# Optimization experiments

Hardware: AMD Instinct MI355X
Metric: run time of the kernel (lower is better)

The kernel has to match this reference:

```python
import jax, jax.numpy as jnp
import numpy as np
from jax import lax

DIM = 192
HEADS = 8
WIN = 16
B, H, W = 4, 256, 256


def setup_inputs() -> dict:
    key = jax.random.key(0)
    ks = jax.random.split(key, 8)
    s = 0.02
    return {
        "x": jax.random.normal(ks[0], (B, H, W, DIM), dtype=jnp.float32),
        "ln_g": jnp.ones((DIM,), jnp.float32),
        "ln_b": jnp.zeros((DIM,), jnp.float32),
        "wq1": jax.random.normal(ks[1], (DIM, DIM), jnp.float32) * s,
        "wq2": jax.random.normal(ks[2], (DIM, 1, 3, 3), jnp.float32) * s,
        "wk1": jax.random.normal(ks[3], (DIM, DIM), jnp.float32) * s,
        "wk2": jax.random.normal(ks[4], (DIM, 1, 3, 3), jnp.float32) * s,
        "wv1": jax.random.normal(ks[5], (DIM, DIM), jnp.float32) * s,
        "wv2": jax.random.normal(ks[6], (DIM, 1, 3, 3), jnp.float32) * s,
        "rescale": jnp.ones((HEADS, 1, 1), jnp.float32),
        "w_out": jax.random.normal(ks[7], (DIM, DIM), jnp.float32) * s,
    }


def _layernorm(x, g, b, eps=1e-5):
    mu = jnp.mean(x, axis=-1, keepdims=True)
    var = jnp.var(x, axis=-1, keepdims=True)
    return (x - mu) * lax.rsqrt(var + eps) * g + b


def _qkv(x_nchw, w1, w2):
    # 1x1 pointwise conv (no bias) as GEMM, then 3x3 depthwise conv (groups=dim)
    y = jnp.einsum('oi,bihw->bohw', w1, x_nchw)
    return lax.conv_general_dilated(
        y, w2, window_strides=(1, 1), padding='SAME',
        feature_group_count=DIM,
        dimension_numbers=('NCHW', 'OIHW', 'NCHW'))


def _windows(t):
    # [b,c,H,W] -> [b, nW, heads, d, n]   (nW = num_h*num_w, n = Wh*Ww)
    b = t.shape[0]
    nh, nw = H // WIN, W // WIN
    t = t.reshape(b, DIM, nh, WIN, nw, WIN)
    t = t.transpose(0, 1, 2, 4, 3, 5).reshape(b, DIM, nh * nw, WIN * WIN)
    d = DIM // HEADS
    t = t.reshape(b, HEADS, d, nh * nw, WIN * WIN)
    return t.transpose(0, 3, 1, 2, 4)  # b N h d n


def reference(x, ln_g, ln_b, wq1, wq2, wk1, wk2, wv1, wv2, rescale, w_out):
    b, h, w, c = x.shape
    xn = _layernorm(x, ln_g, ln_b)
    xc = xn.transpose(0, 3, 1, 2)  # NCHW
    q = _windows(_qkv(xc, wq1, wq2))
    k = _windows(_qkv(xc, wk1, wk2))
    v = _windows(_qkv(xc, wv1, wv2))
    # spectral (channel-wise) attention inside each window
    sim = jnp.einsum('bNhin,bNhjn->bNhij', q, k) * rescale
    attn = jax.nn.softmax(sim, axis=-1)
    out = jnp.einsum('bNhij,bNhjn->bNhin', attn, v)  # [b,N,h,d,n]
    # merge heads, un-window
    nh, nw = h // WIN, w // WIN
    out = out.transpose(0, 2, 3, 1, 4).reshape(b, c, nh * nw, WIN * WIN)
    out = out.reshape(b, c, nh, nw, WIN, WIN).transpose(0, 1, 2, 4, 3, 5).reshape(b, c, h, w)
    out = jnp.einsum('oi,bihw->bohw', w_out, out)
    return out.transpose(0, 2, 3, 1)  # [b,h,w,c]
```

## Files before the change

### kernel.cpp

```cpp
#include <hip/hip_runtime.h>
#include <hip/hip_bf16.h>

#define CH    192
#define NB    4
#define NHH   256
#define NWW   256
#define NPOS  (NB*NHH*NWW)
#define HEADS 8
#define DH    24
#define WIN   16
#define PS    ((size_t)NPOS*DH)

typedef unsigned short u16;
typedef __bf16 bf16x8 __attribute__((ext_vector_type(8)));
typedef float  f32x4  __attribute__((ext_vector_type(4)));
typedef u16    u16x8  __attribute__((ext_vector_type(8)));
typedef u16    u16x4  __attribute__((ext_vector_type(4)));

__device__ __forceinline__ float b2f(u16 h) {
    union { unsigned int u; float f; } x; x.u = ((unsigned int)h) << 16; return x.f;
}
__device__ __forceinline__ u16 f2b(float f) {
    union { float f; unsigned int u; } x; x.f = f;
    return (u16)((x.u + 0x7fffu + ((x.u >> 16) & 1u)) >> 16);
}

__global__ __launch_bounds__(256) void prep_weights(
    const float* __restrict__ w0, const float* __restrict__ w1,
    const float* __restrict__ w2, const float* __restrict__ w3,
    u16* __restrict__ pack)
{
    const int t = blockIdx.x * 256 + threadIdx.x;
    const int lane = t & 63, g = t >> 6;
    const int mat = g / 72;
    const float* w = (mat == 0) ? w0 : (mat == 1) ? w1 : (mat == 2) ? w2 : w3;
    const int nt = (g / 6) % 12, ks = g % 6;
    const float* src = w + (nt*16 + (lane & 15)) * CH + ks*32 + (lane >> 4) * 8;
    const float4 a = *(const float4*)(src);
    const float4 b = *(const float4*)(src + 4);
    u16x8 o;
    o[0]=f2b(a.x); o[1]=f2b(a.y); o[2]=f2b(a.z); o[3]=f2b(a.w);
    o[4]=f2b(b.x); o[5]=f2b(b.y); o[6]=f2b(b.z); o[7]=f2b(b.w);
    *(u16x8*)(pack + (size_t)g*512 + lane*8) = o;
}

__global__ __launch_bounds__(256) void ln_qkv_gemm(
    const float* __restrict__ x, const float* __restrict__ lng, const float* __restrict__ lnb,
    const u16* __restrict__ bpack,
    u16* __restrict__ y0, u16* __restrict__ y1, u16* __restrict__ y2)
{
    __shared__ __align__(16) u16 At[64*192];
    __shared__ __align__(16) u16 St32[32*200];
    const int t = threadIdx.x, l = t & 63, w = t >> 6;
    const int lr = l & 15, lg = l >> 4;
    const size_t p0 = (size_t)blockIdx.x * 64;

    {
        const int row = t >> 2, part = t & 3;
        const float* xp = x + (p0 + row) * CH + part * 48;
        float vals[48];
#pragma unroll
        for (int j = 0; j < 12; ++j) {
            float4 v4 = *(const float4*)(xp + j * 4);
            vals[j*4+0]=v4.x; vals[j*4+1]=v4.y; vals[j*4+2]=v4.z; vals[j*4+3]=v4.w;
        }
        float s = 0.f, s2 = 0.f;
#pragma unroll
        for (int j = 0; j < 48; ++j) { s += vals[j]; s2 += vals[j]*vals[j]; }
        s += __shfl_xor(s, 1);  s2 += __shfl_xor(s2, 1);
        s += __shfl_xor(s, 2);  s2 += __shfl_xor(s2, 2);
        const float mu = s * (1.f/192.f);
        const float rs = rsqrtf(s2 * (1.f/192.f) - mu*mu + 1e-5f);
#pragma unroll
        for (int j8 = 0; j8 < 6; ++j8) {
            u16x8 o;
#pragma unroll
            for (int j = 0; j < 8; ++j) {
                const int c = part*48 + j8*8 + j;
                o[j] = f2b((vals[j8*8+j] - mu) * rs * lng[c] + lnb[c]);
            }
            const int cbs = (part*6 + j8) ^ (row & 7);
            *(u16x8*)&At[row*192 + cbs*8] = o;
        }
    }
    __syncthreads();

    for (int mat = 0; mat < 3; ++mat) {
        u16* yb = (mat == 0) ? y0 : (mat == 1) ? y1 : y2;
        f32x4 acc[4][3];
#pragma unroll
        for (int mt = 0; mt < 4; ++mt)
#pragma unroll
            for (int nt = 0; nt < 3; ++nt) acc[mt][nt] = (f32x4){0.f,0.f,0.f,0.f};
        const u16* bp = bpack + (size_t)mat*36864 + (size_t)w*3*3072 + l*8;
#pragma unroll
        for (int ks = 0; ks < 6; ++ks) {
            bf16x8 wf[3], xf[4];
#pragma unroll
            for (int nt = 0; nt < 3; ++nt)
                wf[nt] = *(const bf16x8*)(bp + (size_t)nt*3072 + ks*512);
#pragma unroll
            for (int mt = 0; mt < 4; ++mt)
                xf[mt] = *(const bf16x8*)&At[(mt*16 + lr)*192 + ((ks*4 + lg) ^ (lr & 7))*8];
#pragma unroll
            for (int mt = 0; mt < 4; ++mt)
#pragma unroll
                for (int nt = 0; nt < 3; ++nt)
                    acc[mt][nt] = __builtin_amdgcn_mfma_f32_16x16x32_bf16(
                        wf[nt], xf[mt], acc[mt][nt], 0, 0, 0);
        }
#pragma unroll
        for (int h2 = 0; h2 < 2; ++h2) {
            __syncthreads();
#pragma unroll
            for (int mi = 0; mi < 2; ++mi) {
                const int mt = h2*2 + mi;
#pragma unroll
                for (int nt = 0; nt < 3; ++nt) {
                    u16x4 pk;
                    pk[0] = f2b(acc[mt][nt][0]); pk[1] = f2b(acc[mt][nt][1]);
                    pk[2] = f2b(acc[mt][nt][2]); pk[3] = f2b(acc[mt][nt][3]);
                    *(u16x4*)&St32[(mi*16 + lr)*200 + (w*3 + nt)*16 + lg*4] = pk;
                }
            }
            __syncthreads();
            const int hh = t >> 5, r = t & 31;
            u16* dst = yb + (size_t)hh*PS + (p0 + h2*32 + r)*DH;
#pragma unroll
            for (int j8 = 0; j8 < 3; ++j8)
                *(u16x8*)(dst + j8*8) = *(const u16x8*)&St32[r*200 + hh*24 + j8*8];
        }
    }
}

__global__ __launch_bounds__(256) void dwconv_kernel(
    const u16* __restrict__ in, const float* __restrict__ wdw, u16* __restrict__ out)
{
    __shared__ float wloc[DH*9];
    const int t = threadIdx.x;
    const int h = blockIdx.y;
    if (t < DH*9) wloc[t] = wdw[h*DH*9 + t];
    __syncthreads();
    const int gid2 = blockIdx.x * 256 + t;
    const int p  = gid2 / 3, c8 = gid2 - p*3;
    const int x = p & 255, y = (p >> 8) & 255, b = p >> 16;
    const size_t plane = (size_t)h * PS;
    float acc[8] = {0,0,0,0,0,0,0,0};
#pragma unroll
    for (int ky = 0; ky < 3; ++ky) {
        const int yy = y + ky - 1;
        if (yy < 0 || yy >= NHH) continue;
#pragma unroll
        for (int kx = 0; kx < 3; ++kx) {
            const int xx = x + kx - 1;
            if (xx < 0 || xx >= NWW) continue;
            const u16x8 iv = *(const u16x8*)(in + plane + (size_t)((b*NHH + yy)*NWW + xx)*DH + c8*8);
#pragma unroll
            for (int j = 0; j < 8; ++j)
                acc[j] += b2f(iv[j]) * wloc[(c8*8 + j)*9 + ky*3 + kx];
        }
    }
    u16x8 ov;
#pragma unroll
    for (int j = 0; j < 8; ++j) ov[j] = f2b(acc[j]);
    *(u16x8*)(out + plane + (size_t)p*DH + c8*8) = ov;
}

__global__ __launch_bounds__(256) void attn_kernel(
    const u16* __restrict__ q, const u16* __restrict__ k, const u16* __restrict__ v,
    const float* __restrict__ rescale, u16* __restrict__ out)
{
    __shared__ float qt[DH][260];
    __shared__ float kt[DH][260];
    float* pbuf = &kt[0][0];
    const int t    = threadIdx.x;
    const int widx = blockIdx.x;
    const int h    = blockIdx.y;
    const int b  = widx >> 8;
    const int wy = (widx >> 4) & 15, wx = widx & 15;
    const int n  = t;
    const int gy = wy*WIN + (n >> 4), gx = wx*WIN + (n & 15);
    const size_t pbase = (size_t)h*PS + (size_t)((b*NHH + gy)*NWW + gx) * DH;

#pragma unroll
    for (int j8 = 0; j8 < 3; ++j8) {
        const u16x8 qv = *(const u16x8*)(q + pbase + j8*8);
        const u16x8 kv = *(const u16x8*)(k + pbase + j8*8);
#pragma unroll
        for (int j = 0; j < 8; ++j) { qt[j8*8+j][n] = b2f(qv[j]); kt[j8*8+j][n] = b2f(kv[j]); }
    }
    __syncthreads();

    const int wvi  = t >> 6;
    const int lane = t & 63;
    const int i0 = (lane >> 3) * 3, j0 = (lane & 7) * 3;
    float s[3][3];
#pragma unroll
    for (int a2 = 0; a2 < 3; ++a2)
#pragma unroll
        for (int c = 0; c < 3; ++c) s[a2][c] = 0.f;
    for (int nn = wvi*64; nn < wvi*64 + 64; nn += 4) {
        float4 qv[3], kv[3];
#pragma unroll
        for (int a2 = 0; a2 < 3; ++a2) {
            qv[a2] = *(const float4*)&qt[i0+a2][nn];
            kv[a2] = *(const float4*)&kt[j0+a2][nn];
        }
#pragma unroll
        for (int a2 = 0; a2 < 3; ++a2)
#pragma unroll
            for (int c = 0; c < 3; ++c)
                s[a2][c] += qv[a2].x*kv[c].x + qv[a2].y*kv[c].y + qv[a2].z*kv[c].z + qv[a2].w*kv[c].w;
    }
    __syncthreads();

#pragma unroll
    for (int a2 = 0; a2 < 3; ++a2)
#pragma unroll
        for (int c = 0; c < 3; ++c)
            pbuf[wvi*576 + (i0+a2)*24 + (j0+c)] = s[a2][c];
#pragma unroll
    for (int j8 = 0; j8 < 3; ++j8) {
        const u16x8 vv = *(const u16x8*)(v + pbase + j8*8);
#pragma unroll
        for (int j = 0; j < 8; ++j) qt[j8*8+j][n] = b2f(vv[j]);
    }
    __syncthreads();

    const float rsc = rescale[h];
    for (int e = t; e < 576; e += 256) {
        const float sum = pbuf[e] + pbuf[576+e] + pbuf[1152+e] + pbuf[1728+e];
        pbuf[2304 + e] = sum * rsc;
    }
    __syncthreads();

    if (t < 24) {
        float* srow = pbuf + 2304 + t*24;
        float m = srow[0];
#pragma unroll
        for (int j = 1; j < 24; ++j) m = fmaxf(m, srow[j]);
        float ssum = 0.f;
#pragma unroll
        for (int j = 0; j < 24; ++j) { const float e_ = expf(srow[j] - m); srow[j] = e_; ssum += e_; }
        const float inv = 1.f / ssum;
#pragma unroll
        for (int j = 0; j < 24; ++j) srow[j] *= inv;
    }
    __syncthreads();

    const int nc = t & 63;
    const int ib = (t >> 6) * 6;
    float4 acc[6];
#pragma unroll
    for (int ii = 0; ii < 6; ++ii) acc[ii] = make_float4(0.f,0.f,0.f,0.f);
#pragma unroll
    for (int j = 0; j < 24; ++j) {
        const float4 vj = *(const float4*)&qt[j][nc*4];
        const float aw0 = pbuf[2304 + (ib+0)*24 + j];
        const float aw1 = pbuf[2304 + (ib+1)*24 + j];
        const float aw2 = pbuf[2304 + (ib+2)*24 + j];
        const float aw3 = pbuf[2304 + (ib+3)*24 + j];
        const float aw4 = pbuf[2304 + (ib+4)*24 + j];
        const float aw5 = pbuf[2304 + (ib+5)*24 + j];
        acc[0].x += aw0*vj.x; acc[0].y += aw0*vj.y; acc[0].z += aw0*vj.z; acc[0].w += aw0*vj.w;
        acc[1].x += aw1*vj.x; acc[1].y += aw1*vj.y; acc[1].z += aw1*vj.z; acc[1].w += aw1*vj.w;
        acc[2].x += aw2*vj.x; acc[2].y += aw2*vj.y; acc[2].z += aw2*vj.z; acc[2].w += aw2*vj.w;
        acc[3].x += aw3*vj.x; acc[3].y += aw3*vj.y; acc[3].z += aw3*vj.z; acc[3].w += aw3*vj.w;
        acc[4].x += aw4*vj.x; acc[4].y += aw4*vj.y; acc[4].z += aw4*vj.z; acc[4].w += aw4*vj.w;
        acc[5].x += aw5*vj.x; acc[5].y += aw5*vj.y; acc[5].z += aw5*vj.z; acc[5].w += aw5*vj.w;
    }
    __syncthreads();
#pragma unroll
    for (int ii = 0; ii < 6; ++ii)
        *(float4*)&qt[ib+ii][nc*4] = acc[ii];
    __syncthreads();
#pragma unroll
    for (int j8 = 0; j8 < 3; ++j8) {
        u16x8 o;
#pragma unroll
        for (int j = 0; j < 8; ++j) o[j] = f2b(qt[j8*8+j][n]);
        *(u16x8*)(out + pbase + j8*8) = o;
    }
}

__global__ __launch_bounds__(256) void outproj_gemm(
    const u16* __restrict__ a, const u16* __restrict__ bpack, float* __restrict__ yf)
{
    __shared__ __align__(16) float St[64][196];
    const int t = threadIdx.x, l = t & 63, w = t >> 6;
    const int lr = l & 15, lg = l >> 4;
    const size_t p0 = (size_t)blockIdx.x * 64;

    f32x4 acc[4][3];
#pragma unroll
    for (int mt = 0; mt < 4; ++mt)
#pragma unroll
        for (int nt = 0; nt < 3; ++nt) acc[mt][nt] = (f32x4){0.f,0.f,0.f,0.f};
    const u16* bp = bpack + (size_t)3*36864 + (size_t)w*3*3072 + l*8;
#pragma unroll
    for (int ks = 0; ks < 6; ++ks) {
        const int ch0 = ks*32 + lg*8;
        const int hh = ch0 / 24, cc = ch0 - hh*24;
        const u16* ap = a + (size_t)hh*PS + (p0 + lr)*DH + cc;
        bf16x8 af[4], bfr[3];
#pragma unroll
        for (int nt = 0; nt < 3; ++nt)
            bfr[nt] = *(const bf16x8*)(bp + (size_t)nt*3072 + ks*512);
#pragma unroll
        for (int mt = 0; mt < 4; ++mt)
            af[mt] = *(const bf16x8*)(ap + (size_t)mt*16*DH);
#pragma unroll
        for (int mt = 0; mt < 4; ++mt)
#pragma unroll
            for (int nt = 0; nt < 3; ++nt)
                acc[mt][nt] = __builtin_amdgcn_mfma_f32_16x16x32_bf16(
                    af[mt], bfr[nt], acc[mt][nt], 0, 0, 0);
    }
#pragma unroll
    for (int mt = 0; mt < 4; ++mt)
#pragma unroll
        for (int nt = 0; nt < 3; ++nt)
#pragma unroll
            for (int reg = 0; reg < 4; ++reg)
                St[mt*16 + lg*4 + reg][(w*3 + nt)*16 + lr] = acc[mt][nt][reg];
    __syncthreads();
#pragma unroll
    for (int i = 0; i < 12; ++i) {
        const int f = t + i*256;
        const int row = f / 48, c4 = f - row*48;
        *(float4*)(yf + (p0 + row)*CH + c4*4) = *(const float4*)&St[row][c4*4];
    }
}

extern "C" void kernel_launch(void* const* d_in, const int* in_sizes, int n_in,
                              void* d_out, int out_size, void* d_ws, size_t ws_size,
                              hipStream_t stream)
{
    (void)in_sizes; (void)n_in; (void)out_size; (void)ws_size;
    const float* x     = (const float*)d_in[0];
    const float* ln_g  = (const float*)d_in[1];
    const float* ln_b  = (const float*)d_in[2];
    const float* wq1   = (const float*)d_in[3];
    const float* wq2   = (const float*)d_in[4];
    const float* wk1   = (const float*)d_in[5];
    const float* wk2   = (const float*)d_in[6];
    const float* wv1   = (const float*)d_in[7];
    const float* wv2   = (const float*)d_in[8];
    const float* rsc   = (const float*)d_in[9];
    const float* w_out = (const float*)d_in[10];
    float* out = (float*)d_out;

    const size_t NT = (size_t)NPOS * CH;
    u16* u1 = (u16*)d_ws;
    u16* u2 = u1 + NT;
    u16* u3 = u2 + NT;
    u16* u4 = u3 + NT;
    u16* pack = u4 + NT;

    prep_weights<<<72, 256, 0, stream>>>(wq1, wk1, wv1, w_out, pack);
    ln_qkv_gemm<<<NPOS/64, 256, 0, stream>>>(x, ln_g, ln_b, pack, u1, u2, u3);
    dwconv_kernel<<<dim3(NPOS*3/256, HEADS), 256, 0, stream>>>(u1, wq2, u4);
    dwconv_kernel<<<dim3(NPOS*3/256, HEADS), 256, 0, stream>>>(u2, wk2, u1);
    dwconv_kernel<<<dim3(NPOS*3/256, HEADS), 256, 0, stream>>>(u3, wv2, u2);
    attn_kernel<<<dim3(NB*256, HEADS), 256, 0, stream>>>(u4, u1, u2, rsc, u3);
    outproj_gemm<<<NPOS/64, 256, 0, stream>>>(u3, pack, out);
}
```

Before: 630.3 us.

## Merge dwconv launches, shrink GEMM staging LDS, stage outproj A via LDS

The three depthwise-conv launches become one kernel indexed by blockIdx.z, writing to extra workspace buffers so the Q, K and V convs can run concurrently. The QKV GEMM epilogue now stages 16 rows at a time instead of 32, which shrinks shared memory and may raise occupancy, at the cost of more barriers and half the threads idling during stores. The out-projection loads its A tile cooperatively into swizzled LDS rather than doing strided per-lane global loads, and stages its fp32 output in two halves to cut LDS use. It needs two more workspace buffers.

After: 602.2 us. -4.5%, faster.

```diff
diff --git a/kernel.cpp b/kernel.cpp
--- a/kernel.cpp
+++ b/kernel.cpp
@@ -50,7 +50,7 @@
     u16* __restrict__ y0, u16* __restrict__ y1, u16* __restrict__ y2)
 {
     __shared__ __align__(16) u16 At[64*192];
-    __shared__ __align__(16) u16 St32[32*200];
+    __shared__ __align__(16) u16 St16[16*200];
     const int t = threadIdx.x, l = t & 63, w = t >> 6;
     const int lr = l & 15, lg = l >> 4;
     const size_t p0 = (size_t)blockIdx.x * 64;
@@ -110,33 +110,37 @@
                         wf[nt], xf[mt], acc[mt][nt], 0, 0, 0);
         }
 #pragma unroll
-        for (int h2 = 0; h2 < 2; ++h2) {
+        for (int hc = 0; hc < 4; ++hc) {
             __syncthreads();
 #pragma unroll
-            for (int mi = 0; mi < 2; ++mi) {
-                const int mt = h2*2 + mi;
-#pragma unroll
-                for (int nt = 0; nt < 3; ++nt) {
-                    u16x4 pk;
-                    pk[0] = f2b(acc[mt][nt][0]); pk[1] = f2b(acc[mt][nt][1]);
-                    pk[2] = f2b(acc[mt][nt][2]); pk[3] = f2b(acc[mt][nt][3]);
-                    *(u16x4*)&St32[(mi*16 + lr)*200 + (w*3 + nt)*16 + lg*4] = pk;
-                }
+            for (int nt = 0; nt < 3; ++nt) {
+                u16x4 pk;
+                pk[0] = f2b(acc[hc][nt][0]); pk[1] = f2b(acc[hc][nt][1]);
+                pk[2] = f2b(acc[hc][nt][2]); pk[3] = f2b(acc[hc][nt][3]);
+                *(u16x4*)&St16[lr*200 + (w*3 + nt)*16 + lg*4] = pk;
             }
             __syncthreads();
-            const int hh = t >> 5, r = t & 31;
-            u16* dst = yb + (size_t)hh*PS + (p0 + h2*32 + r)*DH;
-#pragma unroll
-            for (int j8 = 0; j8 < 3; ++j8)
-                *(u16x8*)(dst + j8*8) = *(const u16x8*)&St32[r*200 + hh*24 + j8*8];
-        }
-    }
-}
-
-__global__ __launch_bounds__(256) void dwconv_kernel(
-    const u16* __restrict__ in, const float* __restrict__ wdw, u16* __restrict__ out)
+            if (t < 128) {
+                const int hh = t >> 4, r = t & 15;
+                u16* dst = yb + (size_t)hh*PS + (p0 + hc*16 + r)*DH;
+#pragma unroll
+                for (int j8 = 0; j8 < 3; ++j8)
+                    *(u16x8*)(dst + j8*8) = *(const u16x8*)&St16[r*200 + hh*24 + j8*8];
+            }
+        }
+    }
+}
+
+__global__ __launch_bounds__(256) void dwconv_all(
+    const u16* __restrict__ in0, const u16* __restrict__ in1, const u16* __restrict__ in2,
+    const float* __restrict__ w0, const float* __restrict__ w1, const float* __restrict__ w2,
+    u16* __restrict__ out0, u16* __restrict__ out1, u16* __restrict__ out2)
 {
     __shared__ float wloc[DH*9];
+    const int z = blockIdx.z;
+    const u16* in  = (z == 0) ? in0  : (z == 1) ? in1  : in2;
+    const float* wdw = (z == 0) ? w0 : (z == 1) ? w1 : w2;
+    u16* out       = (z == 0) ? out0 : (z == 1) ? out1 : out2;
     const int t = threadIdx.x;
     const int h = blockIdx.y;
     if (t < DH*9) wloc[t] = wdw[h*DH*9 + t];
@@ -286,11 +290,23 @@
 __global__ __launch_bounds__(256) void outproj_gemm(
     const u16* __restrict__ a, const u16* __restrict__ bpack, float* __restrict__ yf)
 {
-    __shared__ __align__(16) float St[64][196];
+    __shared__ __align__(16) u16 At[64*192];
+    __shared__ __align__(16) float Sf[32*196];
     const int t = threadIdx.x, l = t & 63, w = t >> 6;
     const int lr = l & 15, lg = l >> 4;
     const size_t p0 = (size_t)blockIdx.x * 64;
 
+#pragma unroll
+    for (int i = 0; i < 6; ++i) {
+        const int idx = t + i*256;
+        const int h = idx / 192;
+        const int rem = idx - h*192;
+        const int r = rem / 3, c8 = rem - r*3;
+        const u16x8 vv = *(const u16x8*)(a + (size_t)h*PS + (p0 + r)*DH + c8*8);
+        *(u16x8*)&At[r*192 + (((h*3 + c8) ^ (r & 7))*8)] = vv;
+    }
+    __syncthreads();
+
     f32x4 acc[4][3];
 #pragma unroll
     for (int mt = 0; mt < 4; ++mt)
@@ -299,16 +315,13 @@
     const u16* bp = bpack + (size_t)3*36864 + (size_t)w*3*3072 + l*8;
 #pragma unroll
     for (int ks = 0; ks < 6; ++ks) {
-        const int ch0 = ks*32 + lg*8;
-        const int hh = ch0 / 24, cc = ch0 - hh*24;
-        const u16* ap = a + (size_t)hh*PS + (p0 + lr)*DH + cc;
         bf16x8 af[4], bfr[3];
 #pragma unroll
         for (int nt = 0; nt < 3; ++nt)
             bfr[nt] = *(const bf16x8*)(bp + (size_t)nt*3072 + ks*512);
 #pragma unroll
         for (int mt = 0; mt < 4; ++mt)
-            af[mt] = *(const bf16x8*)(ap + (size_t)mt*16*DH);
+            af[mt] = *(const bf16x8*)&At[(mt*16 + lr)*192 + ((ks*4 + lg) ^ (lr & 7))*8];
 #pragma unroll
         for (int mt = 0; mt < 4; ++mt)
 #pragma unroll
@@ -317,18 +330,24 @@
                     af[mt], bfr[nt], acc[mt][nt], 0, 0, 0);
     }
 #pragma unroll
-    for (int mt = 0; mt < 4; ++mt)
-#pragma unroll
-        for (int nt = 0; nt < 3; ++nt)
-#pragma unroll
-            for (int reg = 0; reg < 4; ++reg)
-                St[mt*16 + lg*4 + reg][(w*3 + nt)*16 + lr] = acc[mt][nt][reg];
-    __syncthreads();
-#pragma unroll
-    for (int i = 0; i < 12; ++i) {
-        const int f = t + i*256;
-        const int row = f / 48, c4 = f - row*48;
-        *(float4*)(yf + (p0 + row)*CH + c4*4) = *(const float4*)&St[row][c4*4];
+    for (int h2 = 0; h2 < 2; ++h2) {
+        if (h2) __syncthreads();
+#pragma unroll
+        for (int mi = 0; mi < 2; ++mi) {
+            const int mt = h2*2 + mi;
+#pragma unroll
+            for (int nt = 0; nt < 3; ++nt)
+#pragma unroll
+                for (int reg = 0; reg < 4; ++reg)
+                    Sf[(mi*16 + lg*4 + reg)*196 + (w*3 + nt)*16 + lr] = acc[mt][nt][reg];
+        }
+        __syncthreads();
+#pragma unroll
+        for (int i = 0; i < 6; ++i) {
+            const int f = t + i*256;
+            const int row = f / 48, c4 = f - row*48;
+            *(float4*)(yf + (p0 + h2*32 + row)*CH + c4*4) = *(const float4*)&Sf[row*196 + c4*4];
+        }
     }
 }
 
@@ -355,13 +374,14 @@
     u16* u2 = u1 + NT;
     u16* u3 = u2 + NT;
     u16* u4 = u3 + NT;
-    u16* pack = u4 + NT;
+    u16* u5 = u4 + NT;
+    u16* u6 = u5 + NT;
+    u16* pack = u6 + NT;
 
     prep_weights<<<72, 256, 0, stream>>>(wq1, wk1, wv1, w_out, pack);
     ln_qkv_gemm<<<NPOS/64, 256, 0, stream>>>(x, ln_g, ln_b, pack, u1, u2, u3);
-    dwconv_kernel<<<dim3(NPOS*3/256, HEADS), 256, 0, stream>>>(u1, wq2, u4);
-    dwconv_kernel<<<dim3(NPOS*3/256, HEADS), 256, 0, stream>>>(u2, wk2, u1);
-    dwconv_kernel<<<dim3(NPOS*3/256, HEADS), 256, 0, stream>>>(u3, wv2, u2);
-    attn_kernel<<<dim3(NB*256, HEADS), 256, 0, stream>>>(u4, u1, u2, rsc, u3);
-    outproj_gemm<<<NPOS/64, 256, 0, stream>>>(u3, pack, out);
-}
+    dwconv_all<<<dim3(NPOS*3/256, HEADS, 3), 256, 0, stream>>>(
+        u1, u2, u3, wq2, wk2, wv2, u4, u5, u6);
+    attn_kernel<<<dim3(NB*256, HEADS), 256, 0, stream>>>(u4, u5, u6, rsc, u1);
+    outproj_gemm<<<NPOS/64, 256, 0, stream>>>(u1, pack, out);
+}
```
